# Performance work log

Hardware: AMD Instinct MI355X
Metric: run time of the kernel (lower is better)

Reference implementation:

```python
import jax, jax.numpy as jnp
import numpy as np
from jax import lax

DIM = 768
INTER = 512
E = 8            # n_routed_experts
G = 4            # n_expert_groups
TOPK_G = 2       # n_limited_groups
TOPK = 2         # n_activated_experts
ROUTE_SCALE = 1.0


def setup_inputs() -> dict:
    key = jax.random.key(0)
    ks = jax.random.split(key, 9)
    s = 1.0 / np.sqrt(DIM)
    si = 1.0 / np.sqrt(INTER)
    return {
        "x": jax.random.normal(ks[0], (4, 4096, DIM), jnp.float32),
        "gate_weight": jax.random.uniform(ks[1], (E, DIM), jnp.float32, -s, s),
        "gate_bias": jnp.zeros((E,), jnp.float32),
        # stacked routed-expert weights, torch Linear layout [out, in]
        "w1": jax.random.uniform(ks[2], (E, INTER, DIM), jnp.float32, -s, s),
        "w2": jax.random.uniform(ks[3], (E, DIM, INTER), jnp.float32, -si, si),
        "w3": jax.random.uniform(ks[4], (E, INTER, DIM), jnp.float32, -s, s),
        # shared expert (MLP) weights
        "sw1": jax.random.uniform(ks[5], (INTER, DIM), jnp.float32, -s, s),
        "sw2": jax.random.uniform(ks[6], (DIM, INTER), jnp.float32, -si, si),
        "sw3": jax.random.uniform(ks[7], (INTER, DIM), jnp.float32, -s, s),
    }


def _gate(x2, gate_weight, gate_bias):
    # x2: [T, dim]
    T = x2.shape[0]
    scores = jax.nn.sigmoid(x2 @ gate_weight.T)          # [T, E] original scores
    s = scores + gate_bias                               # bias only affects selection
    sv = s.reshape(T, G, E // G)                         # [T, G, E/G]
    top2, _ = lax.top_k(sv, 2)                           # bias path: top-2 per group
    group_scores = top2.sum(-1)                          # [T, G]
    _, gidx = lax.top_k(group_scores, TOPK_G)            # [T, topk_groups]
    gmask = jnp.zeros((T, G), bool).at[jnp.arange(T)[:, None], gidx].set(True)
    masked = jnp.where(gmask[:, :, None], sv, -jnp.inf).reshape(T, E)
    _, idx = lax.top_k(masked, TOPK)                     # [T, topk]
    w = jnp.take_along_axis(scores, idx, axis=1)         # gather from ORIGINAL scores
    w = w / (w.sum(-1, keepdims=True) + 1e-6) * ROUTE_SCALE
    return w, idx


def reference(x, gate_weight, gate_bias, w1, w2, w3, sw1, sw2, sw3):
    B, S, D = x.shape
    x2 = x.reshape(-1, D)                                # [T, D]
    T = x2.shape[0]
    weights, indices = _gate(x2, gate_weight, gate_bias)
    # per-token per-expert combine weight [T, E] (scatter routed weights)
    cw = jnp.zeros((T, E), x.dtype).at[jnp.arange(T)[:, None], indices].add(weights)
    # dense grouped-expert SwiGLU: same math as sparse dispatch
    h1 = jnp.einsum('td,eid->tei', x2, w1)               # [T, E, INTER]
    h3 = jnp.einsum('td,eid->tei', x2, w3)
    h = jax.nn.silu(h1) * h3
    y = jnp.einsum('tei,edi,te->td', h, w2, cw)          # combine
    # shared expert MLP
    z = (jax.nn.silu(x2 @ sw1.T) * (x2 @ sw3.T)) @ sw2.T
    return (y + z).reshape(B, S, D)
```

## Files before the change

### kernel.cpp

```cpp
#include <hip/hip_runtime.h>
#include <math.h>

#define DIM_  768
#define INT_  512
#define NE    8
#define MROWS 48
#define PERMAT 393216

typedef unsigned int u32;
typedef unsigned short u16;
typedef __attribute__((ext_vector_type(4))) u32   u32x4;
typedef __attribute__((ext_vector_type(8))) short bf16x8;
typedef __attribute__((ext_vector_type(4))) float f32x4;

#define MFMA(acc, a, b) acc = __builtin_amdgcn_mfma_f32_16x16x32_bf16(a, b, acc, 0, 0, 0)

static __device__ __forceinline__ u16 f2bf(float f) {
  u32 u = __builtin_bit_cast(u32, f);
  return (u16)((u + 0x7fffu + ((u >> 16) & 1u)) >> 16);
}
static __device__ __forceinline__ float bf2f(u16 s) {
  u32 u = ((u32)s) << 16; return __builtin_bit_cast(float, u);
}
template<int L>
static __device__ __forceinline__ int swoff(int row, int wi) {
  int g = (wi >> 2) ^ ((row & 7) << 1);
  return row * L + ((g & (L / 4 - 1)) << 2) + (wi & 3);
}

__global__ __launch_bounds__(256)
void gate_kernel(const float* __restrict__ x, const float* __restrict__ gw,
                 const float* __restrict__ gb, int* __restrict__ pidx,
                 float* __restrict__ wgt, int* __restrict__ bh, int T) {
  __shared__ int hist[16];
  const int tid = threadIdx.x;
  if (tid < 16) hist[tid] = 0;
  __syncthreads();
  const int t = blockIdx.x * 256 + tid;
  if (t < T) {
    float acc[NE] = {};
    const float* xr = x + (size_t)t * DIM_;
    for (int k0 = 0; k0 < DIM_; k0 += 8) {
      float4 xa = *(const float4*)&xr[k0];
      float4 xb = *(const float4*)&xr[k0 + 4];
#pragma unroll
      for (int e = 0; e < NE; ++e) {
        const float* g8 = &gw[e * DIM_ + k0];
        acc[e] = fmaf(xa.x, g8[0], acc[e]);
        acc[e] = fmaf(xa.y, g8[1], acc[e]);
        acc[e] = fmaf(xa.z, g8[2], acc[e]);
        acc[e] = fmaf(xa.w, g8[3], acc[e]);
        acc[e] = fmaf(xb.x, g8[4], acc[e]);
        acc[e] = fmaf(xb.y, g8[5], acc[e]);
        acc[e] = fmaf(xb.z, g8[6], acc[e]);
        acc[e] = fmaf(xb.w, g8[7], acc[e]);
      }
    }
    float sc[NE], s[NE];
#pragma unroll
    for (int e = 0; e < NE; ++e) {
      sc[e] = 1.0f / (1.0f + expf(-acc[e]));
      s[e]  = sc[e] + gb[e];
    }
    float gsc[4];
#pragma unroll
    for (int g = 0; g < 4; ++g) gsc[g] = s[2*g] + s[2*g+1];
    int g1 = 0; float b1v = gsc[0];
#pragma unroll
    for (int g = 1; g < 4; ++g) if (gsc[g] > b1v) { b1v = gsc[g]; g1 = g; }
    int g2 = (g1 == 0) ? 1 : 0;
    float b2v = (g1 == 0) ? gsc[1] : gsc[0];
#pragma unroll
    for (int g = 0; g < 4; ++g)
      if ((g != g1) && (gsc[g] > b2v)) { b2v = gsc[g]; g2 = g; }
    unsigned mask = (3u << (2*g1)) | (3u << (2*g2));
    int e1 = -1; float bs1 = -3.0e38f;
#pragma unroll
    for (int e = 0; e < NE; ++e) {
      bool in = (mask >> e) & 1u;
      if (in && (s[e] > bs1)) { bs1 = s[e]; e1 = e; }
    }
    int e2 = -1; float bs2 = -3.0e38f;
#pragma unroll
    for (int e = 0; e < NE; ++e) {
      bool in = ((mask >> e) & 1u) && (e != e1);
      if (in && (s[e] > bs2)) { bs2 = s[e]; e2 = e; }
    }
    float wa = 0.f, wb = 0.f;
#pragma unroll
    for (int e = 0; e < NE; ++e) {
      if (e == e1) wa = sc[e];
      if (e == e2) wb = sc[e];
    }
    float inv = 1.0f / (wa + wb + 1e-6f);
    wa *= inv; wb *= inv;
    pidx[t] = e1 | (e2 << 8);
    wgt[2*t] = wa; wgt[2*t+1] = wb;
    atomicAdd(&hist[e1], 1);
    atomicAdd(&hist[8 + e2], 1);
  }
  __syncthreads();
  if (tid < 16) bh[blockIdx.x * 16 + tid] = hist[tid];
}

__global__ void scan_kernel(int* __restrict__ bh, int* __restrict__ cnt,
                            int* __restrict__ offs, int NB) {
  __shared__ int colsum[16], base_s[16];
  const int tid = threadIdx.x;
  if (tid < 16) {
    int s = 0;
    for (int b = 0; b < NB; ++b) {
      int v = bh[b * 16 + tid];
      bh[b * 16 + tid] = s;
      s += v;
    }
    colsum[tid] = s;
  }
  __syncthreads();
  if (tid == 0) {
    int a = 0;
    for (int L = 0; L < 16; ++L) {
      base_s[L] = a; offs[L] = a; cnt[L] = colsum[L]; a += colsum[L];
    }
  }
  __syncthreads();
  if (tid < 16) {
    int add = base_s[tid];
    for (int b = 0; b < NB; ++b) bh[b * 16 + tid] += add;
  }
}

__global__ __launch_bounds__(256)
void scatter_kernel(const int* __restrict__ pidx, const float* __restrict__ wgt,
                    const int* __restrict__ bh, int* __restrict__ tok,
                    float* __restrict__ wof, int T) {
  __shared__ int lcur[16];
  const int tid = threadIdx.x;
  if (tid < 16) lcur[tid] = bh[blockIdx.x * 16 + tid];
  __syncthreads();
  const int t = blockIdx.x * 256 + tid;
  if (t < T) {
    int pi = pidx[t];
    int e1 = pi & 255, e2 = (pi >> 8) & 255;
    int p0 = atomicAdd(&lcur[e1], 1);
    tok[p0] = t; wof[p0] = wgt[2*t];
    int p1 = atomicAdd(&lcur[8 + e2], 1);
    tok[p1] = t; wof[p1] = wgt[2*t+1];
  }
}

__global__ __launch_bounds__(256)
void prep_kernel(const float* __restrict__ w1, const float* __restrict__ w3,
                 const float* __restrict__ w2, const float* __restrict__ sw1,
                 const float* __restrict__ sw3, const float* __restrict__ sw2,
                 u32* __restrict__ P1, u32* __restrict__ P3, u32* __restrict__ P2) {
  const int PER = 9 * 768 * 64;
  int gid = blockIdx.x * 256 + threadIdx.x;
  int which = gid / PER;
  int r = gid % PER;
  int lane = r & 63;
  int fe = r >> 6;
  int fs = fe % 768;
  int e  = fe / 768;
  int c16 = lane & 15, q = lane >> 4;

  const float* src; u32* dst;
  if (which < 2) {
    int nb = fs / 24, ks = fs % 24;
    int col = nb * 16 + c16, k0 = ks * 32 + q * 8;
    const float* wm = (which == 0) ? w1 : w3;
    const float* sm = (which == 0) ? sw1 : sw3;
    src = (e < 8) ? wm + ((size_t)e * INT_ + col) * DIM_ + k0
                  : sm + (size_t)col * DIM_ + k0;
    dst = ((which == 0) ? P1 : P3) + ((size_t)(e * 768 + fs) * 64 + lane) * 8;
  } else {
    int nb = fs / 16, ks = fs % 16;
    int col = nb * 16 + c16, k0 = ks * 32 + q * 8;
    src = (e < 8) ? w2 + ((size_t)e * DIM_ + col) * INT_ + k0
                  : sw2 + (size_t)col * INT_ + k0;
    dst = P2 + ((size_t)(e * 768 + fs) * 64 + lane) * 8;
  }
  float4 a = *(const float4*)src;
  float4 b = *(const float4*)(src + 4);
  u16 h0=f2bf(a.x), h1=f2bf(a.y), h2=f2bf(a.z), h3=f2bf(a.w);
  u16 h4=f2bf(b.x), h5=f2bf(b.y), h6=f2bf(b.z), h7=f2bf(b.w);
  u32x4 H = { (u32)h0|((u32)h1<<16), (u32)h2|((u32)h3<<16),
              (u32)h4|((u32)h5<<16), (u32)h6|((u32)h7<<16) };
  u32x4 Lv = { (u32)f2bf(a.x-bf2f(h0)) | ((u32)f2bf(a.y-bf2f(h1))<<16),
               (u32)f2bf(a.z-bf2f(h2)) | ((u32)f2bf(a.w-bf2f(h3))<<16),
               (u32)f2bf(b.x-bf2f(h4)) | ((u32)f2bf(b.y-bf2f(h5))<<16),
               (u32)f2bf(b.z-bf2f(h6)) | ((u32)f2bf(b.w-bf2f(h7))<<16) };
  *(u32x4*)dst = H;
  *(u32x4*)(dst + 4) = Lv;
}

template<bool SHARED>
__global__ __launch_bounds__(512, 2)
void expert_mfma(const float* __restrict__ x,
                 const u32* __restrict__ P1, const u32* __restrict__ P3,
                 const u32* __restrict__ P2,
                 const int* __restrict__ cnt, const int* __restrict__ offs,
                 const int* __restrict__ tok, const float* __restrict__ wof,
                 float* __restrict__ out, int T, int slot, int tpe, int nwg) {
  extern __shared__ u32 sm[];
  u32* Xh = sm;
  u32* Xl = Xh + 6144;
  u32* Hh = Xl + 6144;
  u32* Hl = Hh + 12288;
  int*   rts_s = (int*)(Hl + 12288);
  float* wrs_s = (float*)(rts_s + MROWS);

  int orig = blockIdx.x;
  int q8 = nwg >> 3, rr = nwg & 7, xcd = orig & 7, pos = orig >> 3;
  int wgid = (xcd < rr ? xcd * (q8 + 1) : rr * (q8 + 1) + (xcd - rr) * q8) + pos;

  int e, n, off0, tile;
  if (SHARED) { e = 8; tile = wgid; n = T; off0 = 0; }
  else {
    e = wgid / tpe; tile = wgid % tpe;
    int L = slot * 8 + e;
    n = cnt[L]; off0 = offs[L];
  }
  const int r0 = tile * MROWS;
  if (r0 >= n) return;
  const int nr = min(MROWS, n - r0);
  const int tid = threadIdx.x;

  if (tid < MROWS) {
    int r = r0 + tid;
    if (SHARED) { rts_s[tid] = min(r, T - 1); wrs_s[tid] = 1.0f; }
    else {
      int rc = min(r, n - 1);
      rts_s[tid] = tok[off0 + rc];
      wrs_s[tid] = (r < n) ? wof[off0 + r] : 0.0f;
    }
  }
  __syncthreads();

  const int lane = tid & 63, wid = tid >> 6;
  const int c16 = lane & 15, q = lane >> 4;
  const u32* P1e = P1 + (size_t)e * PERMAT;
  const u32* P3e = P3 + (size_t)e * PERMAT;
  const u32* P2e = P2 + (size_t)e * PERMAT;

  f32x4 acc1[3][4] = {};
  f32x4 acc3[3][4] = {};
  for (int ch = 0; ch < 3; ++ch) {
    __syncthreads();
    {
      const int cb = ch * 256;
#pragma unroll
      for (int u = 0; u < 6; ++u) {
        int f = u * 512 + tid;
        int row = f >> 6, kq = f & 63;
        float4 v = *(const float4*)&x[(size_t)rts_s[row] * DIM_ + cb + kq * 4];
        u16 a0 = f2bf(v.x), a1 = f2bf(v.y), a2 = f2bf(v.z), a3 = f2bf(v.w);
        int base = swoff<128>(row, kq * 2);
        Xh[base]     = (u32)a0 | ((u32)a1 << 16);
        Xh[base + 1] = (u32)a2 | ((u32)a3 << 16);
        Xl[base]     = (u32)f2bf(v.x - bf2f(a0)) | ((u32)f2bf(v.y - bf2f(a1)) << 16);
        Xl[base + 1] = (u32)f2bf(v.z - bf2f(a2)) | ((u32)f2bf(v.w - bf2f(a3)) << 16);
      }
    }
    __syncthreads();
    for (int ks = 0; ks < 8; ++ks) {
      bf16x8 Ah[3], Al[3];
#pragma unroll
      for (int m = 0; m < 3; ++m) {
        int row = 16 * m + c16;
        int wi = ks * 16 + q * 4;
        Ah[m] = __builtin_bit_cast(bf16x8, *(const u32x4*)&Xh[swoff<128>(row, wi)]);
        Al[m] = __builtin_bit_cast(bf16x8, *(const u32x4*)&Xl[swoff<128>(row, wi)]);
      }
      const int gks = ch * 8 + ks;
#pragma unroll
      for (int nf = 0; nf < 4; ++nf) {
        int nb = wid * 4 + nf;
        const u32* p1 = P1e + ((size_t)(nb * 24 + gks) * 64 + lane) * 8;
        const u32* p3 = P3e + ((size_t)(nb * 24 + gks) * 64 + lane) * 8;
        bf16x8 B1h = __builtin_bit_cast(bf16x8, *(const u32x4*)p1);
        bf16x8 B1l = __builtin_bit_cast(bf16x8, *(const u32x4*)(p1 + 4));
        bf16x8 B3h = __builtin_bit_cast(bf16x8, *(const u32x4*)p3);
        bf16x8 B3l = __builtin_bit_cast(bf16x8, *(const u32x4*)(p3 + 4));
#pragma unroll
        for (int m = 0; m < 3; ++m) {
          MFMA(acc1[m][nf], Ah[m], B1h);
          MFMA(acc1[m][nf], Al[m], B1h);
          MFMA(acc1[m][nf], Ah[m], B1l);
          MFMA(acc3[m][nf], Ah[m], B3h);
          MFMA(acc3[m][nf], Al[m], B3h);
          MFMA(acc3[m][nf], Ah[m], B3l);
        }
      }
    }
  }
  {
    u16* Hh16 = (u16*)Hh;
    u16* Hl16 = (u16*)Hl;
#pragma unroll
    for (int m = 0; m < 3; ++m)
#pragma unroll
      for (int nf = 0; nf < 4; ++nf)
#pragma unroll
        for (int reg = 0; reg < 4; ++reg) {
          int tokr = 16 * m + 4 * q + reg;
          int col  = (wid * 4 + nf) * 16 + c16;
          float v1 = acc1[m][nf][reg], v3 = acc3[m][nf][reg];
          float h = v1 / (1.0f + expf(-v1)) * v3;
          u16 hh = f2bf(h);
          u16 hl = f2bf(h - bf2f(hh));
          int wo = swoff<256>(tokr, col >> 1);
          Hh16[wo * 2 + (col & 1)] = hh;
          Hl16[wo * 2 + (col & 1)] = hl;
        }
  }
  __syncthreads();

  f32x4 acc2[3][6] = {};
  for (int ks = 0; ks < 16; ++ks) {
    bf16x8 Ah[3], Al[3];
#pragma unroll
    for (int m = 0; m < 3; ++m) {
      int row = 16 * m + c16;
      int wi = ks * 16 + q * 4;
      Ah[m] = __builtin_bit_cast(bf16x8, *(const u32x4*)&Hh[swoff<256>(row, wi)]);
      Al[m] = __builtin_bit_cast(bf16x8, *(const u32x4*)&Hl[swoff<256>(row, wi)]);
    }
#pragma unroll
    for (int nf = 0; nf < 6; ++nf) {
      int nb = wid * 6 + nf;
      const u32* p2 = P2e + ((size_t)(nb * 16 + ks) * 64 + lane) * 8;
      bf16x8 Bh = __builtin_bit_cast(bf16x8, *(const u32x4*)p2);
      bf16x8 Bl = __builtin_bit_cast(bf16x8, *(const u32x4*)(p2 + 4));
#pragma unroll
      for (int m = 0; m < 3; ++m) {
        MFMA(acc2[m][nf], Ah[m], Bh);
        MFMA(acc2[m][nf], Al[m], Bh);
        MFMA(acc2[m][nf], Ah[m], Bl);
      }
    }
  }
#pragma unroll
  for (int m = 0; m < 3; ++m)
#pragma unroll
    for (int reg = 0; reg < 4; ++reg) {
      int tr = 16 * m + 4 * q + reg;
      if (tr < nr) {
        int gt = rts_s[tr];
        float wv = wrs_s[tr];
        float* po = out + (size_t)gt * DIM_ + c16;
#pragma unroll
        for (int nf = 0; nf < 6; ++nf) {
          int col = (wid * 6 + nf) * 16;
          float val = acc2[m][nf][reg] * wv;
          if (SHARED) po[col] = val;
          else        po[col] += val;
        }
      }
    }
}

extern "C" void kernel_launch(void* const* d_in, const int* in_sizes, int n_in,
                              void* d_out, int out_size, void* d_ws, size_t ws_size,
                              hipStream_t stream) {
  const float* x   = (const float*)d_in[0];
  const float* gw  = (const float*)d_in[1];
  const float* gb  = (const float*)d_in[2];
  const float* w1  = (const float*)d_in[3];
  const float* w2  = (const float*)d_in[4];
  const float* w3  = (const float*)d_in[5];
  const float* sw1 = (const float*)d_in[6];
  const float* sw2 = (const float*)d_in[7];
  const float* sw3 = (const float*)d_in[8];
  float* out = (float*)d_out;
  const int T = in_sizes[0] / DIM_;
  const int NB = (T + 255) / 256;

  u32* P1 = (u32*)d_ws;
  u32* P3 = P1 + (size_t)9 * PERMAT;
  u32* P2 = P3 + (size_t)9 * PERMAT;
  int*   bh   = (int*)(P2 + (size_t)9 * PERMAT);
  int*   cnt  = bh + NB * 16;
  int*   offs = cnt + 16;
  int*   pidx = offs + 16;
  float* wgt  = (float*)(pidx + T);
  int*   tokl = (int*)(wgt + 2 * T);
  float* wof  = (float*)(tokl + 2 * T);

  const size_t smem = (size_t)(2 * 6144 + 2 * 12288 + MROWS + MROWS) * 4;
  hipFuncSetAttribute(reinterpret_cast<const void*>(expert_mfma<true>),
                      hipFuncAttributeMaxDynamicSharedMemorySize, (int)smem);
  hipFuncSetAttribute(reinterpret_cast<const void*>(expert_mfma<false>),
                      hipFuncAttributeMaxDynamicSharedMemorySize, (int)smem);

  prep_kernel<<<5184, 256, 0, stream>>>(w1, w3, w2, sw1, sw3, sw2, P1, P3, P2);
  gate_kernel<<<NB, 256, 0, stream>>>(x, gw, gb, pidx, wgt, bh, T);
  scan_kernel<<<1, 64, 0, stream>>>(bh, cnt, offs, NB);
  scatter_kernel<<<NB, 256, 0, stream>>>(pidx, wgt, bh, tokl, wof, T);

  const int tpe = (T + MROWS - 1) / MROWS;
  expert_mfma<true ><<<tpe, 512, smem, stream>>>(x, P1, P3, P2,
      nullptr, nullptr, nullptr, nullptr, out, T, 0, tpe, tpe);
  expert_mfma<false><<<NE * tpe, 512, smem, stream>>>(x, P1, P3, P2,
      cnt, offs, tokl, wof, out, T, 0, tpe, NE * tpe);
  expert_mfma<false><<<NE * tpe, 512, smem, stream>>>(x, P1, P3, P2,
      cnt, offs, tokl, wof, out, T, 1, tpe, NE * tpe);
}
```

Baseline: 662.0 us.

## Shrink expert tiles to 32 rows with finer K staging for higher occupancy

Reduces the token tile from 48 to 32 rows and stages x in 64-column chunks over 12 iterations instead of 256-column chunks over 3. This cuts LDS use from about 147KB to about 74KB and raises launch bounds to 4 blocks per CU. The XOR swizzle is replaced by a simpler rotate-by-row layout. The goal is more resident waves to hide global weight-load latency. In exchange, each weight fragment is reused across fewer rows, so weight traffic per token rises, and there are more barriers per block.

```diff
diff --git a/kernel.cpp b/kernel.cpp
--- a/kernel.cpp
+++ b/kernel.cpp
@@ -4,11 +4,12 @@
 #define DIM_  768
 #define INT_  512
 #define NE    8
-#define MROWS 48
+#define MROWS 32
 #define PERMAT 393216
 
 typedef unsigned int u32;
 typedef unsigned short u16;
+typedef __attribute__((ext_vector_type(2))) u32   u32x2;
 typedef __attribute__((ext_vector_type(4))) u32   u32x4;
 typedef __attribute__((ext_vector_type(8))) short bf16x8;
 typedef __attribute__((ext_vector_type(4))) float f32x4;
@@ -21,11 +22,6 @@
 }
 static __device__ __forceinline__ float bf2f(u16 s) {
   u32 u = ((u32)s) << 16; return __builtin_bit_cast(float, u);
-}
-template<int L>
-static __device__ __forceinline__ int swoff(int row, int wi) {
-  int g = (wi >> 2) ^ ((row & 7) << 1);
-  return row * L + ((g & (L / 4 - 1)) << 2) + (wi & 3);
 }
 
 __global__ __launch_bounds__(256)
@@ -195,7 +191,7 @@
 }
 
 template<bool SHARED>
-__global__ __launch_bounds__(512, 2)
+__global__ __launch_bounds__(512, 4)
 void expert_mfma(const float* __restrict__ x,
                  const u32* __restrict__ P1, const u32* __restrict__ P3,
                  const u32* __restrict__ P2,
@@ -204,10 +200,10 @@
                  float* __restrict__ out, int T, int slot, int tpe, int nwg) {
   extern __shared__ u32 sm[];
   u32* Xh = sm;
-  u32* Xl = Xh + 6144;
-  u32* Hh = Xl + 6144;
-  u32* Hl = Hh + 12288;
-  int*   rts_s = (int*)(Hl + 12288);
+  u32* Xl = Xh + 1024;
+  u32* Hh = Xl + 1024;
+  u32* Hl = Hh + 8192;
+  int*   rts_s = (int*)(Hl + 8192);
   float* wrs_s = (float*)(rts_s + MROWS);
 
   int orig = blockIdx.x;
@@ -243,36 +239,36 @@
   const u32* P3e = P3 + (size_t)e * PERMAT;
   const u32* P2e = P2 + (size_t)e * PERMAT;
 
-  f32x4 acc1[3][4] = {};
-  f32x4 acc3[3][4] = {};
-  for (int ch = 0; ch < 3; ++ch) {
+  const int srow = tid >> 4;
+  const float* xrow = x + (size_t)rts_s[srow] * DIM_ + (tid & 15) * 4;
+  const int swb = (tid & 15) * 2;
+  const int sws = srow * 32 + ((swb + 4 * srow) & 31);
+
+  f32x4 acc1[2][4] = {};
+  f32x4 acc3[2][4] = {};
+  for (int kc = 0; kc < 12; ++kc) {
     __syncthreads();
     {
-      const int cb = ch * 256;
-#pragma unroll
-      for (int u = 0; u < 6; ++u) {
-        int f = u * 512 + tid;
-        int row = f >> 6, kq = f & 63;
-        float4 v = *(const float4*)&x[(size_t)rts_s[row] * DIM_ + cb + kq * 4];
-        u16 a0 = f2bf(v.x), a1 = f2bf(v.y), a2 = f2bf(v.z), a3 = f2bf(v.w);
-        int base = swoff<128>(row, kq * 2);
-        Xh[base]     = (u32)a0 | ((u32)a1 << 16);
-        Xh[base + 1] = (u32)a2 | ((u32)a3 << 16);
-        Xl[base]     = (u32)f2bf(v.x - bf2f(a0)) | ((u32)f2bf(v.y - bf2f(a1)) << 16);
-        Xl[base + 1] = (u32)f2bf(v.z - bf2f(a2)) | ((u32)f2bf(v.w - bf2f(a3)) << 16);
+      float4 v = *(const float4*)(xrow + kc * 64);
+      u16 a0 = f2bf(v.x), a1 = f2bf(v.y), a2 = f2bf(v.z), a3 = f2bf(v.w);
+      u32x2 Hp = { (u32)a0 | ((u32)a1 << 16), (u32)a2 | ((u32)a3 << 16) };
+      u32x2 Lp = { (u32)f2bf(v.x - bf2f(a0)) | ((u32)f2bf(v.y - bf2f(a1)) << 16),
+                   (u32)f2bf(v.z - bf2f(a2)) | ((u32)f2bf(v.w - bf2f(a3)) << 16) };
+      *(u32x2*)&Xh[sws] = Hp;
+      *(u32x2*)&Xl[sws] = Lp;
+    }
+    __syncthreads();
+#pragma unroll
+    for (int gl = 0; gl < 2; ++gl) {
+      const int gks = kc * 2 + gl;
+      bf16x8 Ah[2], Al[2];
+#pragma unroll
+      for (int m = 0; m < 2; ++m) {
+        int row = 16 * m + c16;
+        int wb = row * 32 + ((gl * 16 + q * 4 + 4 * row) & 31);
+        Ah[m] = __builtin_bit_cast(bf16x8, *(const u32x4*)&Xh[wb]);
+        Al[m] = __builtin_bit_cast(bf16x8, *(const u32x4*)&Xl[wb]);
       }
-    }
-    __syncthreads();
-    for (int ks = 0; ks < 8; ++ks) {
-      bf16x8 Ah[3], Al[3];
-#pragma unroll
-      for (int m = 0; m < 3; ++m) {
-        int row = 16 * m + c16;
-        int wi = ks * 16 + q * 4;
-        Ah[m] = __builtin_bit_cast(bf16x8, *(const u32x4*)&Xh[swoff<128>(row, wi)]);
-        Al[m] = __builtin_bit_cast(bf16x8, *(const u32x4*)&Xl[swoff<128>(row, wi)]);
-      }
-      const int gks = ch * 8 + ks;
 #pragma unroll
       for (int nf = 0; nf < 4; ++nf) {
         int nb = wid * 4 + nf;
@@ -283,7 +279,7 @@
         bf16x8 B3h = __builtin_bit_cast(bf16x8, *(const u32x4*)p3);
         bf16x8 B3l = __builtin_bit_cast(bf16x8, *(const u32x4*)(p3 + 4));
 #pragma unroll
-        for (int m = 0; m < 3; ++m) {
+        for (int m = 0; m < 2; ++m) {
           MFMA(acc1[m][nf], Ah[m], B1h);
           MFMA(acc1[m][nf], Al[m], B1h);
           MFMA(acc1[m][nf], Ah[m], B1l);
@@ -298,7 +294,7 @@
     u16* Hh16 = (u16*)Hh;
     u16* Hl16 = (u16*)Hl;
 #pragma unroll
-    for (int m = 0; m < 3; ++m)
+    for (int m = 0; m < 2; ++m)
 #pragma unroll
       for (int nf = 0; nf < 4; ++nf)
 #pragma unroll
@@ -309,22 +305,23 @@
           float h = v1 / (1.0f + expf(-v1)) * v3;
           u16 hh = f2bf(h);
           u16 hl = f2bf(h - bf2f(hh));
-          int wo = swoff<256>(tokr, col >> 1);
-          Hh16[wo * 2 + (col & 1)] = hh;
-          Hl16[wo * 2 + (col & 1)] = hl;
+          int w  = col >> 1;
+          int wr = tokr * 256 + ((w + 4 * tokr) & 255);
+          Hh16[wr * 2 + (col & 1)] = hh;
+          Hl16[wr * 2 + (col & 1)] = hl;
         }
   }
   __syncthreads();
 
-  f32x4 acc2[3][6] = {};
+  f32x4 acc2[2][6] = {};
   for (int ks = 0; ks < 16; ++ks) {
-    bf16x8 Ah[3], Al[3];
-#pragma unroll
-    for (int m = 0; m < 3; ++m) {
+    bf16x8 Ah[2], Al[2];
+#pragma unroll
+    for (int m = 0; m < 2; ++m) {
       int row = 16 * m + c16;
-      int wi = ks * 16 + q * 4;
-      Ah[m] = __builtin_bit_cast(bf16x8, *(const u32x4*)&Hh[swoff<256>(row, wi)]);
-      Al[m] = __builtin_bit_cast(bf16x8, *(const u32x4*)&Hl[swoff<256>(row, wi)]);
+      int wb = row * 256 + ((ks * 16 + q * 4 + 4 * row) & 255);
+      Ah[m] = __builtin_bit_cast(bf16x8, *(const u32x4*)&Hh[wb]);
+      Al[m] = __builtin_bit_cast(bf16x8, *(const u32x4*)&Hl[wb]);
     }
 #pragma unroll
     for (int nf = 0; nf < 6; ++nf) {
@@ -333,7 +330,7 @@
       bf16x8 Bh = __builtin_bit_cast(bf16x8, *(const u32x4*)p2);
       bf16x8 Bl = __builtin_bit_cast(bf16x8, *(const u32x4*)(p2 + 4));
 #pragma unroll
-      for (int m = 0; m < 3; ++m) {
+      for (int m = 0; m < 2; ++m) {
         MFMA(acc2[m][nf], Ah[m], Bh);
         MFMA(acc2[m][nf], Al[m], Bh);
         MFMA(acc2[m][nf], Ah[m], Bl);
@@ -341,7 +338,7 @@
     }
   }
 #pragma unroll
-  for (int m = 0; m < 3; ++m)
+  for (int m = 0; m < 2; ++m)
 #pragma unroll
     for (int reg = 0; reg < 4; ++reg) {
       int tr = 16 * m + 4 * q + reg;
@@ -387,7 +384,7 @@
   int*   tokl = (int*)(wgt + 2 * T);
   float* wof  = (float*)(tokl + 2 * T);
 
-  const size_t smem = (size_t)(2 * 6144 + 2 * 12288 + MROWS + MROWS) * 4;
+  const size_t smem = (size_t)(2 * 1024 + 2 * 8192 + MROWS + MROWS) * 4;
   hipFuncSetAttribute(reinterpret_cast<const void*>(expert_mfma<true>),
                       hipFuncAttributeMaxDynamicSharedMemorySize, (int)smem);
   hipFuncSetAttribute(reinterpret_cast<const void*>(expert_mfma<false>),
```

New measurement: 799.3 us. 1.21x slower.
